# Performance work log

Measured on AMD Instinct MI355X. Metric: run time of the kernel, lower is better.

Reference implementation:

```python
import jax, jax.numpy as jnp
import numpy as np

D = 2          # spatial / tensor dimension (k=1 vector images)
GROUPS = 8     # channel groups
EPS = 1e-05


def setup_inputs() -> dict:
    key = jax.random.key(0)
    kx, kb = jax.random.split(key)
    x = jax.random.normal(kx, (16, 64, 128, 128, D), dtype=jnp.float32)
    scale = jnp.ones((64, 1, 1, 1), dtype=jnp.float32)
    bias = jax.random.normal(kb, (64, 1, 1, 1), dtype=jnp.float32)
    return {"x": x, "scale": scale, "bias": bias}


def reference(x, scale, bias):
    # x: (batch, channels, H, W, D) vector (k=1) image block
    batch, in_c = x.shape[:2]
    spatial = x.shape[2:2 + D]
    cpg = in_c // GROUPS  # channels per group

    # mean vector over spatial dims only, per (batch, channel): (b, c, 1, 1, D)
    mean_vec = jnp.mean(x, axis=tuple(range(2, 2 + D)), keepdims=True)

    # group channels: (b, g, cpg, H, W, D)
    xg = x.reshape((batch, GROUPS, cpg) + spatial + (D,))
    # mean over (cpg, H, W) per group, keeping the D tensor axis
    mean = jnp.mean(xg, axis=tuple(range(2, 3 + D)), keepdims=True)
    centered = xg - mean

    # flatten to (b, g, n, D) with n = cpg*H*W
    Xf = centered.reshape(batch, GROUPS, -1, D)
    n = Xf.shape[2]
    # per-group DxD covariance
    cov = jnp.einsum('bgnj,bgnk->bgjk', Xf, Xf) / n

    # whitening via symmetric eigendecomposition (equivariant, unlike cholesky)
    eigvals, eigvecs = jnp.linalg.eigh(cov, symmetrize_input=False)
    s = jnp.sqrt(1.0 / (eigvals + EPS))  # (b, g, D)
    # W = V diag(s) V^T  (same math as the original chained einsum)
    Wm = jnp.einsum('bgij,bgj,bgkj->bgik', eigvecs, s, eigvecs)
    whitened = jnp.einsum('bgik,bgnk->bgni', Wm, Xf).reshape(x.shape)

    # equivariant affine: scale * whitened + bias * (spatial mean vector)
    return whitened * scale + bias * mean_vec
```

## Files before the change

kernel.cpp:

```cpp
#include <hip/hip_runtime.h>

#define BATCH 16
#define CH 64
#define NGROUPS 8
#define CPG 8
#define HWPIX (128*128)
#define DD 2
#define EPSV 1e-5f
#define SPLIT 4
#define SPLITN 4
#define TPB 256


__global__ __launch_bounds__(TPB) void gn_stats(const float* __restrict__ x,
                                                float* __restrict__ partials) {
    const int blk = blockIdx.x;
    const int sp  = blk % SPLIT;
    const int bc  = blk / SPLIT;
    const int F4_PER_CH = HWPIX * DD / 4;
    const int CHUNK     = F4_PER_CH / SPLIT;
    const float4* base = (const float4*)x + (size_t)bc * F4_PER_CH + (size_t)sp * CHUNK;
    const int tid = threadIdx.x;

    float s0 = 0.f, s1 = 0.f, sxx = 0.f, sxy = 0.f, syy = 0.f;
    const int PER_THREAD = CHUNK / TPB;
#pragma unroll
    for (int i = 0; i < PER_THREAD; ++i) {
        float4 v = base[tid + i * TPB];
        s0 += v.x + v.z;
        s1 += v.y + v.w;
        sxx = fmaf(v.x, v.x, fmaf(v.z, v.z, sxx));
        sxy = fmaf(v.x, v.y, fmaf(v.z, v.w, sxy));
        syy = fmaf(v.y, v.y, fmaf(v.w, v.w, syy));
    }
#pragma unroll
    for (int off = 32; off > 0; off >>= 1) {
        s0  += __shfl_down(s0, off);
        s1  += __shfl_down(s1, off);
        sxx += __shfl_down(sxx, off);
        sxy += __shfl_down(sxy, off);
        syy += __shfl_down(syy, off);
    }
    __shared__ float red[4][5];
    const int wave = tid >> 6, lane = tid & 63;
    if (lane == 0) {
        red[wave][0] = s0; red[wave][1] = s1; red[wave][2] = sxx;
        red[wave][3] = sxy; red[wave][4] = syy;
    }
    __syncthreads();
    if (tid == 0) {
        float r0 = 0.f, r1 = 0.f, r2 = 0.f, r3 = 0.f, r4 = 0.f;
#pragma unroll
        for (int w = 0; w < 4; ++w) {
            r0 += red[w][0]; r1 += red[w][1]; r2 += red[w][2];
            r3 += red[w][3]; r4 += red[w][4];
        }
        float* p = partials + (size_t)(bc * SPLIT + sp) * 5;
        p[0] = r0; p[1] = r1; p[2] = r2; p[3] = r3; p[4] = r4;
    }
}

__global__ void gn_solve(const float* __restrict__ partials,
                         float* __restrict__ solved,
                         float* __restrict__ mv) {
    const int tid = blockIdx.x * blockDim.x + threadIdx.x;
    if (tid < BATCH * CH) {
        float m0 = 0.f, m1 = 0.f;
#pragma unroll
        for (int s = 0; s < SPLIT; ++s) {
            const float* p = partials + ((size_t)tid * SPLIT + s) * 5;
            m0 += p[0]; m1 += p[1];
        }
        mv[tid * 2 + 0] = m0 / (float)HWPIX;
        mv[tid * 2 + 1] = m1 / (float)HWPIX;
    }
    if (tid < BATCH * NGROUPS) {
        const int b = tid / NGROUPS, g = tid % NGROUPS;
        float S0 = 0.f, S1 = 0.f, Sxx = 0.f, Sxy = 0.f, Syy = 0.f;
        for (int c = 0; c < CPG; ++c) {
            const int ch = b * CH + g * CPG + c;
#pragma unroll
            for (int s = 0; s < SPLIT; ++s) {
                const float* p = partials + ((size_t)ch * SPLIT + s) * 5;
                S0 += p[0]; S1 += p[1]; Sxx += p[2]; Sxy += p[3]; Syy += p[4];
            }
        }
        const float n = (float)(CPG * HWPIX);
        const float m0 = S0 / n, m1 = S1 / n;
        const float a  = Sxx / n - m0 * m0 + EPSV;
        const float bq = Sxy / n - m0 * m1;
        const float cc = Syy / n - m1 * m1 + EPSV;
        const float det  = a * cc - bq * bq;
        const float sdet = sqrtf(det);
        const float t    = sqrtf(a + cc + 2.0f * sdet);
        const float inv  = 1.0f / (sdet * t);
        float* so = solved + (size_t)tid * 5;
        so[0] = m0;
        so[1] = m1;
        so[2] = (cc + sdet) * inv;
        so[3] = -bq * inv;
        so[4] = (a + sdet) * inv;
    }
}

__global__ __launch_bounds__(TPB) void gn_norm(const float* __restrict__ x,
                                               const float* __restrict__ solved,
                                               const float* __restrict__ mv,
                                               const float* __restrict__ scale,
                                               const float* __restrict__ bias,
                                               float* __restrict__ out) {
    const int blk = blockIdx.x;
    const int sp  = blk % SPLITN;
    const int bc  = blk / SPLITN;
    const int c   = bc % CH;
    const int b   = bc / CH;
    const int g   = c / CPG;

    const float* so = solved + (size_t)(b * NGROUPS + g) * 5;
    const float m0 = so[0], m1 = so[1];
    const float w00 = so[2], w01 = so[3], w11 = so[4];
    const float sc = scale[c], bi = bias[c];
    const float mv0 = mv[bc * 2 + 0], mv1 = mv[bc * 2 + 1];

    const float a00 = sc * w00, a01 = sc * w01, a11 = sc * w11;
    const float add0 = fmaf(bi, mv0, -(a00 * m0 + a01 * m1));
    const float add1 = fmaf(bi, mv1, -(a01 * m0 + a11 * m1));

    const int F4_PER_CH = HWPIX * DD / 4;
    const int CHUNK     = F4_PER_CH / SPLITN;
    const float4* src = (const float4*)x   + (size_t)bc * F4_PER_CH + (size_t)sp * CHUNK;
    float4*       dst = (float4*)out       + (size_t)bc * F4_PER_CH + (size_t)sp * CHUNK;
    const int tid = threadIdx.x;
    const int PER_THREAD = CHUNK / TPB;
#pragma unroll
    for (int i = 0; i < PER_THREAD; ++i) {
        float4 v = src[tid + i * TPB];
        float4 o;
        o.x = fmaf(a00, v.x, fmaf(a01, v.y, add0));
        o.y = fmaf(a01, v.x, fmaf(a11, v.y, add1));
        o.z = fmaf(a00, v.z, fmaf(a01, v.w, add0));
        o.w = fmaf(a01, v.z, fmaf(a11, v.w, add1));
        dst[tid + i * TPB] = o;
    }
}

extern "C" void kernel_launch(void* const* d_in, const int* in_sizes, int n_in,
                              void* d_out, int out_size, void* d_ws, size_t ws_size,
                              hipStream_t stream) {
    const float* x     = (const float*)d_in[0];
    const float* scale = (const float*)d_in[1];
    const float* bias  = (const float*)d_in[2];
    float* out = (float*)d_out;

    float* partials = (float*)d_ws;
    float* solved   = partials + BATCH * CH * SPLIT * 5;
    float* mv       = solved + BATCH * NGROUPS * 5;

    gn_stats<<<BATCH * CH * SPLIT, TPB, 0, stream>>>(x, partials);
    gn_solve<<<(BATCH * CH + 255) / 256, 256, 0, stream>>>(partials, solved, mv);
    gn_norm<<<BATCH * CH * SPLITN, TPB, 0, stream>>>(x, solved, mv, scale, bias, out);
}
```

Baseline: 69.42 us.

## Fold group solve into normalize kernel and prefetch inputs before coefficient computation

Removes the separate gn_solve launch. Each gn_norm block now reduces the 32 partial stat records of its group with wave shuffles and computes the whitening and affine coefficients into shared memory. The block's input vectors are loaded into registers before that computation so the load latency overlaps the solve. Output is written with nontemporal stores. In exchange, every block repeats the small group solve and holds more registers.

```diff
diff --git a/kernel.cpp b/kernel.cpp
--- a/kernel.cpp
+++ b/kernel.cpp
@@ -11,6 +11,8 @@
 #define SPLITN 4
 #define TPB 256
 
+typedef float fx4 __attribute__((ext_vector_type(4)));
+
 
 __global__ __launch_bounds__(TPB) void gn_stats(const float* __restrict__ x,
                                                 float* __restrict__ partials) {
@@ -19,14 +21,14 @@
     const int bc  = blk / SPLIT;
     const int F4_PER_CH = HWPIX * DD / 4;
     const int CHUNK     = F4_PER_CH / SPLIT;
-    const float4* base = (const float4*)x + (size_t)bc * F4_PER_CH + (size_t)sp * CHUNK;
+    const fx4* base = (const fx4*)x + (size_t)bc * F4_PER_CH + (size_t)sp * CHUNK;
     const int tid = threadIdx.x;
 
     float s0 = 0.f, s1 = 0.f, sxx = 0.f, sxy = 0.f, syy = 0.f;
     const int PER_THREAD = CHUNK / TPB;
 #pragma unroll
     for (int i = 0; i < PER_THREAD; ++i) {
-        float4 v = base[tid + i * TPB];
+        fx4 v = base[tid + i * TPB];
         s0 += v.x + v.z;
         s1 += v.y + v.w;
         sxx = fmaf(v.x, v.x, fmaf(v.z, v.z, sxx));
@@ -60,52 +62,8 @@
     }
 }
 
-__global__ void gn_solve(const float* __restrict__ partials,
-                         float* __restrict__ solved,
-                         float* __restrict__ mv) {
-    const int tid = blockIdx.x * blockDim.x + threadIdx.x;
-    if (tid < BATCH * CH) {
-        float m0 = 0.f, m1 = 0.f;
-#pragma unroll
-        for (int s = 0; s < SPLIT; ++s) {
-            const float* p = partials + ((size_t)tid * SPLIT + s) * 5;
-            m0 += p[0]; m1 += p[1];
-        }
-        mv[tid * 2 + 0] = m0 / (float)HWPIX;
-        mv[tid * 2 + 1] = m1 / (float)HWPIX;
-    }
-    if (tid < BATCH * NGROUPS) {
-        const int b = tid / NGROUPS, g = tid % NGROUPS;
-        float S0 = 0.f, S1 = 0.f, Sxx = 0.f, Sxy = 0.f, Syy = 0.f;
-        for (int c = 0; c < CPG; ++c) {
-            const int ch = b * CH + g * CPG + c;
-#pragma unroll
-            for (int s = 0; s < SPLIT; ++s) {
-                const float* p = partials + ((size_t)ch * SPLIT + s) * 5;
-                S0 += p[0]; S1 += p[1]; Sxx += p[2]; Sxy += p[3]; Syy += p[4];
-            }
-        }
-        const float n = (float)(CPG * HWPIX);
-        const float m0 = S0 / n, m1 = S1 / n;
-        const float a  = Sxx / n - m0 * m0 + EPSV;
-        const float bq = Sxy / n - m0 * m1;
-        const float cc = Syy / n - m1 * m1 + EPSV;
-        const float det  = a * cc - bq * bq;
-        const float sdet = sqrtf(det);
-        const float t    = sqrtf(a + cc + 2.0f * sdet);
-        const float inv  = 1.0f / (sdet * t);
-        float* so = solved + (size_t)tid * 5;
-        so[0] = m0;
-        so[1] = m1;
-        so[2] = (cc + sdet) * inv;
-        so[3] = -bq * inv;
-        so[4] = (a + sdet) * inv;
-    }
-}
-
 __global__ __launch_bounds__(TPB) void gn_norm(const float* __restrict__ x,
-                                               const float* __restrict__ solved,
-                                               const float* __restrict__ mv,
+                                               const float* __restrict__ partials,
                                                const float* __restrict__ scale,
                                                const float* __restrict__ bias,
                                                float* __restrict__ out) {
@@ -115,32 +73,70 @@
     const int c   = bc % CH;
     const int b   = bc / CH;
     const int g   = c / CPG;
-
-    const float* so = solved + (size_t)(b * NGROUPS + g) * 5;
-    const float m0 = so[0], m1 = so[1];
-    const float w00 = so[2], w01 = so[3], w11 = so[4];
-    const float sc = scale[c], bi = bias[c];
-    const float mv0 = mv[bc * 2 + 0], mv1 = mv[bc * 2 + 1];
-
-    const float a00 = sc * w00, a01 = sc * w01, a11 = sc * w11;
-    const float add0 = fmaf(bi, mv0, -(a00 * m0 + a01 * m1));
-    const float add1 = fmaf(bi, mv1, -(a01 * m0 + a11 * m1));
+    const int cig = c % CPG;
 
     const int F4_PER_CH = HWPIX * DD / 4;
     const int CHUNK     = F4_PER_CH / SPLITN;
-    const float4* src = (const float4*)x   + (size_t)bc * F4_PER_CH + (size_t)sp * CHUNK;
-    float4*       dst = (float4*)out       + (size_t)bc * F4_PER_CH + (size_t)sp * CHUNK;
+    const fx4* src = (const fx4*)x + (size_t)bc * F4_PER_CH + (size_t)sp * CHUNK;
+    fx4*       dst = (fx4*)out     + (size_t)bc * F4_PER_CH + (size_t)sp * CHUNK;
     const int tid = threadIdx.x;
     const int PER_THREAD = CHUNK / TPB;
+
+    fx4 v[PER_THREAD];
+#pragma unroll
+    for (int i = 0; i < PER_THREAD; ++i) v[i] = src[tid + i * TPB];
+
+    __shared__ float coef[5];
+    if (tid < 32) {
+        const float* p = partials +
+            ((size_t)(b * CH + g * CPG + (tid >> 2)) * SPLIT + (tid & 3)) * 5;
+        float p0 = p[0], p1 = p[1], p2 = p[2], p3 = p[3], p4 = p[4];
+        const bool mine = (tid >> 2) == cig;
+        float q0 = mine ? p0 : 0.f, q1 = mine ? p1 : 0.f;
+#pragma unroll
+        for (int off = 16; off > 0; off >>= 1) {
+            p0 += __shfl_xor(p0, off, 32);
+            p1 += __shfl_xor(p1, off, 32);
+            p2 += __shfl_xor(p2, off, 32);
+            p3 += __shfl_xor(p3, off, 32);
+            p4 += __shfl_xor(p4, off, 32);
+            q0 += __shfl_xor(q0, off, 32);
+            q1 += __shfl_xor(q1, off, 32);
+        }
+        if (tid == 0) {
+            const float n  = (float)(CPG * HWPIX);
+            const float m0 = p0 / n, m1 = p1 / n;
+            const float a  = p2 / n - m0 * m0 + EPSV;
+            const float bq = p3 / n - m0 * m1;
+            const float cc = p4 / n - m1 * m1 + EPSV;
+            const float sdet = sqrtf(a * cc - bq * bq);
+            const float t    = sqrtf(a + cc + 2.0f * sdet);
+            const float inv  = 1.0f / (sdet * t);
+            const float w00 = (cc + sdet) * inv;
+            const float w01 = -bq * inv;
+            const float w11 = (a + sdet) * inv;
+            const float sc = scale[c], bi = bias[c];
+            const float mv0 = q0 / (float)HWPIX, mv1 = q1 / (float)HWPIX;
+            const float a00 = sc * w00, a01 = sc * w01, a11 = sc * w11;
+            coef[0] = a00;
+            coef[1] = a01;
+            coef[2] = a11;
+            coef[3] = fmaf(bi, mv0, -(a00 * m0 + a01 * m1));
+            coef[4] = fmaf(bi, mv1, -(a01 * m0 + a11 * m1));
+        }
+    }
+    __syncthreads();
+    const float a00 = coef[0], a01 = coef[1], a11 = coef[2];
+    const float add0 = coef[3], add1 = coef[4];
+
 #pragma unroll
     for (int i = 0; i < PER_THREAD; ++i) {
-        float4 v = src[tid + i * TPB];
-        float4 o;
-        o.x = fmaf(a00, v.x, fmaf(a01, v.y, add0));
-        o.y = fmaf(a01, v.x, fmaf(a11, v.y, add1));
-        o.z = fmaf(a00, v.z, fmaf(a01, v.w, add0));
-        o.w = fmaf(a01, v.z, fmaf(a11, v.w, add1));
-        dst[tid + i * TPB] = o;
+        fx4 o;
+        o.x = fmaf(a00, v[i].x, fmaf(a01, v[i].y, add0));
+        o.y = fmaf(a01, v[i].x, fmaf(a11, v[i].y, add1));
+        o.z = fmaf(a00, v[i].z, fmaf(a01, v[i].w, add0));
+        o.w = fmaf(a01, v[i].z, fmaf(a11, v[i].w, add1));
+        __builtin_nontemporal_store(o, &dst[tid + i * TPB]);
     }
 }
 
@@ -153,10 +149,7 @@
     float* out = (float*)d_out;
 
     float* partials = (float*)d_ws;
-    float* solved   = partials + BATCH * CH * SPLIT * 5;
-    float* mv       = solved + BATCH * NGROUPS * 5;
 
     gn_stats<<<BATCH * CH * SPLIT, TPB, 0, stream>>>(x, partials);
-    gn_solve<<<(BATCH * CH + 255) / 256, 256, 0, stream>>>(partials, solved, mv);
-    gn_norm<<<BATCH * CH * SPLITN, TPB, 0, stream>>>(x, solved, mv, scale, bias, out);
+    gn_norm<<<BATCH * CH * SPLITN, TPB, 0, stream>>>(x, partials, scale, bias, out);
 }
```

Result: faster. 64.39 us (-7.2%).
